# Kernel optimization log

Measured on AMD Instinct MI355X. Metric: run time of the kernel, lower is better.

## Reference

```python
import jax, jax.numpy as jnp
import numpy as np

N_ATOMS = 200_000
N_EDGES = 6_400_000  # ~32 neighbors/atom at 6A cutoff


def setup_inputs() -> dict:
    key = jax.random.key(0)
    k1, k2, k3, k4 = jax.random.split(key, 4)
    box_len = 60.0  # cubic cell edge (Angstrom) holding ~200k atoms
    pos = jax.random.uniform(k1, (N_ATOMS, 3), dtype=jnp.float32) * box_len
    # slightly triclinic periodic cell, batch of 1 structure
    box = (jnp.eye(3, dtype=jnp.float32) * box_len
           + jax.random.normal(k2, (3, 3), dtype=jnp.float32) * 0.5)[None]  # [1,3,3]
    edge_index = jax.random.randint(k3, (2, N_EDGES), 0, N_ATOMS, dtype=jnp.int32)
    shifts_idx = jax.random.randint(k4, (N_EDGES, 3), 0, 3, dtype=jnp.int32) - 1  # in {-1,0,1}
    batch_map = jnp.zeros((N_EDGES,), dtype=jnp.int32)  # single structure
    return {"pos": pos, "box": box, "edge_index": edge_index,
            "shifts_idx": shifts_idx, "batch_map": batch_map}


def reference(pos, box, edge_index, shifts_idx, batch_map):
    # compute_cell_shifts: per-edge shift vector = shifts_idx @ cell[batch]
    shifts_f = shifts_idx.astype(pos.dtype)                      # [E,3]
    cell_shifts = jnp.einsum('en,enm->em', shifts_f, box[batch_map])  # [E,3]
    # compute_distances + edge_vec (gather-based, periodic-corrected)
    dr = pos[edge_index[1]] - pos[edge_index[0]] + cell_shifts   # [E,3]
    edge_weight = jnp.linalg.norm(dr, axis=1)                    # [E]
    edge_vec = -dr                                               # [E,3]
    return edge_index, edge_weight, edge_vec, shifts_idx
```

## Files before the change

kernel.cpp:

```cpp
#include <hip/hip_runtime.h>


typedef int   vint4   __attribute__((ext_vector_type(4)));
typedef float vfloat4 __attribute__((ext_vector_type(4)));

struct f3 { float x, y, z; };

template <bool MULTI>
__global__ __launch_bounds__(256) void pd_kernel(
    const float* __restrict__ pos,
    const float* __restrict__ box,
    const int*   __restrict__ ei,
    const int*   __restrict__ sh,
    const int*   __restrict__ bmap,
    float* __restrict__ out,
    const long long E)
{
    const long long nG = E >> 2;
    float* out_ei = out;
    float* out_w  = out + 2 * E;
    float* out_v  = out + 3 * E;
    float* out_s  = out + 6 * E;

    float b00, b01, b02, b10, b11, b12, b20, b21, b22;
    if (!MULTI) {
        b00 = box[0]; b01 = box[1]; b02 = box[2];
        b10 = box[3]; b11 = box[4]; b12 = box[5];
        b20 = box[6]; b21 = box[7]; b22 = box[8];
    }

    const long long stride = (long long)gridDim.x * blockDim.x;

    for (long long g = (long long)blockIdx.x * blockDim.x + threadIdx.x;
         g < nG; g += stride) {
        const long long e0 = g << 2;

        const vint4 i4 = __builtin_nontemporal_load(
            reinterpret_cast<const vint4*>(ei + e0));
        const vint4 j4 = __builtin_nontemporal_load(
            reinterpret_cast<const vint4*>(ei + E + e0));
        const vint4 sA = __builtin_nontemporal_load(
            reinterpret_cast<const vint4*>(sh + 3 * e0));
        const vint4 sB = __builtin_nontemporal_load(
            reinterpret_cast<const vint4*>(sh + 3 * e0 + 4));
        const vint4 sC = __builtin_nontemporal_load(
            reinterpret_cast<const vint4*>(sh + 3 * e0 + 8));

        {
            vfloat4 t;
            t = (vfloat4){(float)i4.x, (float)i4.y, (float)i4.z, (float)i4.w};
            __builtin_nontemporal_store(t, reinterpret_cast<vfloat4*>(out_ei + e0));
            t = (vfloat4){(float)j4.x, (float)j4.y, (float)j4.z, (float)j4.w};
            __builtin_nontemporal_store(t, reinterpret_cast<vfloat4*>(out_ei + E + e0));
            t = (vfloat4){(float)sA.x, (float)sA.y, (float)sA.z, (float)sA.w};
            __builtin_nontemporal_store(t, reinterpret_cast<vfloat4*>(out_s + 3 * e0));
            t = (vfloat4){(float)sB.x, (float)sB.y, (float)sB.z, (float)sB.w};
            __builtin_nontemporal_store(t, reinterpret_cast<vfloat4*>(out_s + 3 * e0 + 4));
            t = (vfloat4){(float)sC.x, (float)sC.y, (float)sC.z, (float)sC.w};
            __builtin_nontemporal_store(t, reinterpret_cast<vfloat4*>(out_s + 3 * e0 + 8));
        }

        const int iv[4] = {i4.x, i4.y, i4.z, i4.w};
        const int jv[4] = {j4.x, j4.y, j4.z, j4.w};
        const int sv[12] = {sA.x, sA.y, sA.z, sA.w,
                            sB.x, sB.y, sB.z, sB.w,
                            sC.x, sC.y, sC.z, sC.w};
        int bv[4] = {0, 0, 0, 0};
        if (MULTI) {
            const vint4 b4 = __builtin_nontemporal_load(
                reinterpret_cast<const vint4*>(bmap + e0));
            bv[0] = b4.x; bv[1] = b4.y; bv[2] = b4.z; bv[3] = b4.w;
        }

        f3 pjv[4], piv[4];
#pragma unroll
        for (int k = 0; k < 4; ++k) {
            piv[k] = *reinterpret_cast<const f3*>(pos + 3LL * iv[k]);
            pjv[k] = *reinterpret_cast<const f3*>(pos + 3LL * jv[k]);
        }

        float w[4], v[12];
#pragma unroll
        for (int k = 0; k < 4; ++k) {
            float B00, B01, B02, B10, B11, B12, B20, B21, B22;
            if (MULTI) {
                const float* bb = box + 9LL * bv[k];
                B00 = bb[0]; B01 = bb[1]; B02 = bb[2];
                B10 = bb[3]; B11 = bb[4]; B12 = bb[5];
                B20 = bb[6]; B21 = bb[7]; B22 = bb[8];
            } else {
                B00 = b00; B01 = b01; B02 = b02;
                B10 = b10; B11 = b11; B12 = b12;
                B20 = b20; B21 = b21; B22 = b22;
            }
            const float sx = (float)sv[3 * k + 0];
            const float sy = (float)sv[3 * k + 1];
            const float sz = (float)sv[3 * k + 2];
            const float cx = sx * B00 + sy * B10 + sz * B20;
            const float cy = sx * B01 + sy * B11 + sz * B21;
            const float cz = sx * B02 + sy * B12 + sz * B22;

            const float dx = pjv[k].x - piv[k].x + cx;
            const float dy = pjv[k].y - piv[k].y + cy;
            const float dz = pjv[k].z - piv[k].z + cz;

            w[k] = sqrtf(dx * dx + dy * dy + dz * dz);
            v[3 * k + 0] = -dx;
            v[3 * k + 1] = -dy;
            v[3 * k + 2] = -dz;
        }

        __builtin_nontemporal_store(
            (vfloat4){w[0], w[1], w[2], w[3]},
            reinterpret_cast<vfloat4*>(out_w + e0));
        __builtin_nontemporal_store(
            (vfloat4){v[0], v[1], v[2], v[3]},
            reinterpret_cast<vfloat4*>(out_v + 3 * e0));
        __builtin_nontemporal_store(
            (vfloat4){v[4], v[5], v[6], v[7]},
            reinterpret_cast<vfloat4*>(out_v + 3 * e0 + 4));
        __builtin_nontemporal_store(
            (vfloat4){v[8], v[9], v[10], v[11]},
            reinterpret_cast<vfloat4*>(out_v + 3 * e0 + 8));
    }

    const long long tail0 = nG << 2;
    for (long long e = tail0 + (long long)blockIdx.x * blockDim.x + threadIdx.x;
         e < E; e += stride) {
        const int i = ei[e];
        const int j = ei[E + e];
        const int s0 = sh[3 * e], s1 = sh[3 * e + 1], s2 = sh[3 * e + 2];
        out_ei[e]     = (float)i;
        out_ei[E + e] = (float)j;
        out_s[3 * e]     = (float)s0;
        out_s[3 * e + 1] = (float)s1;
        out_s[3 * e + 2] = (float)s2;

        float B00, B01, B02, B10, B11, B12, B20, B21, B22;
        if (MULTI) {
            const float* bb = box + 9LL * bmap[e];
            B00 = bb[0]; B01 = bb[1]; B02 = bb[2];
            B10 = bb[3]; B11 = bb[4]; B12 = bb[5];
            B20 = bb[6]; B21 = bb[7]; B22 = bb[8];
        } else {
            B00 = b00; B01 = b01; B02 = b02;
            B10 = b10; B11 = b11; B12 = b12;
            B20 = b20; B21 = b21; B22 = b22;
        }
        const float sx = (float)s0, sy = (float)s1, sz = (float)s2;
        const float cx = sx * B00 + sy * B10 + sz * B20;
        const float cy = sx * B01 + sy * B11 + sz * B21;
        const float cz = sx * B02 + sy * B12 + sz * B22;
        const float dx = pos[3LL * j + 0] - pos[3LL * i + 0] + cx;
        const float dy = pos[3LL * j + 1] - pos[3LL * i + 1] + cy;
        const float dz = pos[3LL * j + 2] - pos[3LL * i + 2] + cz;
        out_w[e] = sqrtf(dx * dx + dy * dy + dz * dz);
        out_v[3 * e + 0] = -dx;
        out_v[3 * e + 1] = -dy;
        out_v[3 * e + 2] = -dz;
    }
}

extern "C" void kernel_launch(void* const* d_in, const int* in_sizes, int n_in,
                              void* d_out, int out_size, void* d_ws, size_t ws_size,
                              hipStream_t stream) {
    const float* pos  = (const float*)d_in[0];
    const float* box  = (const float*)d_in[1];
    const int*   ei   = (const int*)d_in[2];
    const int*   sh   = (const int*)d_in[3];
    const int*   bmap = (const int*)d_in[4];
    float* out = (float*)d_out;

    const long long E = (long long)in_sizes[4];
    const int n_struct = in_sizes[1] / 9;

    const int block = 256;
    long long nG = (E + 3) >> 2;
    long long blocks = (nG + block - 1) / block;
    if (blocks < 1) blocks = 1;
    if (blocks > 32768) blocks = 32768;

    if (n_struct == 1) {
        pd_kernel<false><<<(int)blocks, block, 0, stream>>>(
            pos, box, ei, sh, bmap, out, E);
    } else {
        pd_kernel<true><<<(int)blocks, block, 0, stream>>>(
            pos, box, ei, sh, bmap, out, E);
    }
}
```

Baseline: 371.1 us.

## Stage vector and shift outputs through LDS for fully coalesced stores

```diff
diff --git a/kernel.cpp b/kernel.cpp
--- a/kernel.cpp
+++ b/kernel.cpp
@@ -6,8 +6,12 @@
 
 struct f3 { float x, y, z; };
 
+#define BLOCK 256
+#define EPT   4
+#define EPB   (BLOCK * EPT)
+
 template <bool MULTI>
-__global__ __launch_bounds__(256) void pd_kernel(
+__global__ __launch_bounds__(BLOCK) void pd_kernel(
     const float* __restrict__ pos,
     const float* __restrict__ box,
     const int*   __restrict__ ei,
@@ -16,11 +20,15 @@
     float* __restrict__ out,
     const long long E)
 {
-    const long long nG = E >> 2;
+    __shared__ float lds[EPB * 3];
+
     float* out_ei = out;
     float* out_w  = out + 2 * E;
     float* out_v  = out + 3 * E;
     float* out_s  = out + 6 * E;
+
+    const int tid = threadIdx.x;
+    const long long E0 = (long long)blockIdx.x * EPB;
 
     float b00, b01, b02, b10, b11, b12, b20, b21, b22;
     if (!MULTI) {
@@ -29,42 +37,34 @@
         b20 = box[6]; b21 = box[7]; b22 = box[8];
     }
 
-    const long long stride = (long long)gridDim.x * blockDim.x;
-
-    for (long long g = (long long)blockIdx.x * blockDim.x + threadIdx.x;
-         g < nG; g += stride) {
-        const long long e0 = g << 2;
+    if (E0 + EPB <= E) {
+        const long long e0 = E0 + (long long)tid * EPT;
 
         const vint4 i4 = __builtin_nontemporal_load(
             reinterpret_cast<const vint4*>(ei + e0));
         const vint4 j4 = __builtin_nontemporal_load(
             reinterpret_cast<const vint4*>(ei + E + e0));
+        const int iv[4] = {i4.x, i4.y, i4.z, i4.w};
+        const int jv[4] = {j4.x, j4.y, j4.z, j4.w};
+
+        f3 piv[4], pjv[4];
+#pragma unroll
+        for (int k = 0; k < 4; ++k) {
+            piv[k] = *reinterpret_cast<const f3*>(pos + 3LL * iv[k]);
+            pjv[k] = *reinterpret_cast<const f3*>(pos + 3LL * jv[k]);
+        }
+
         const vint4 sA = __builtin_nontemporal_load(
             reinterpret_cast<const vint4*>(sh + 3 * e0));
         const vint4 sB = __builtin_nontemporal_load(
             reinterpret_cast<const vint4*>(sh + 3 * e0 + 4));
         const vint4 sC = __builtin_nontemporal_load(
             reinterpret_cast<const vint4*>(sh + 3 * e0 + 8));
-
-        {
-            vfloat4 t;
-            t = (vfloat4){(float)i4.x, (float)i4.y, (float)i4.z, (float)i4.w};
-            __builtin_nontemporal_store(t, reinterpret_cast<vfloat4*>(out_ei + e0));
-            t = (vfloat4){(float)j4.x, (float)j4.y, (float)j4.z, (float)j4.w};
-            __builtin_nontemporal_store(t, reinterpret_cast<vfloat4*>(out_ei + E + e0));
-            t = (vfloat4){(float)sA.x, (float)sA.y, (float)sA.z, (float)sA.w};
-            __builtin_nontemporal_store(t, reinterpret_cast<vfloat4*>(out_s + 3 * e0));
-            t = (vfloat4){(float)sB.x, (float)sB.y, (float)sB.z, (float)sB.w};
-            __builtin_nontemporal_store(t, reinterpret_cast<vfloat4*>(out_s + 3 * e0 + 4));
-            t = (vfloat4){(float)sC.x, (float)sC.y, (float)sC.z, (float)sC.w};
-            __builtin_nontemporal_store(t, reinterpret_cast<vfloat4*>(out_s + 3 * e0 + 8));
-        }
-
-        const int iv[4] = {i4.x, i4.y, i4.z, i4.w};
-        const int jv[4] = {j4.x, j4.y, j4.z, j4.w};
-        const int sv[12] = {sA.x, sA.y, sA.z, sA.w,
-                            sB.x, sB.y, sB.z, sB.w,
-                            sC.x, sC.y, sC.z, sC.w};
+        const float sf[12] = {
+            (float)sA.x, (float)sA.y, (float)sA.z, (float)sA.w,
+            (float)sB.x, (float)sB.y, (float)sB.z, (float)sB.w,
+            (float)sC.x, (float)sC.y, (float)sC.z, (float)sC.w};
+
         int bv[4] = {0, 0, 0, 0};
         if (MULTI) {
             const vint4 b4 = __builtin_nontemporal_load(
@@ -72,12 +72,12 @@
             bv[0] = b4.x; bv[1] = b4.y; bv[2] = b4.z; bv[3] = b4.w;
         }
 
-        f3 pjv[4], piv[4];
-#pragma unroll
-        for (int k = 0; k < 4; ++k) {
-            piv[k] = *reinterpret_cast<const f3*>(pos + 3LL * iv[k]);
-            pjv[k] = *reinterpret_cast<const f3*>(pos + 3LL * jv[k]);
-        }
+        __builtin_nontemporal_store(
+            (vfloat4){(float)i4.x, (float)i4.y, (float)i4.z, (float)i4.w},
+            reinterpret_cast<vfloat4*>(out_ei + e0));
+        __builtin_nontemporal_store(
+            (vfloat4){(float)j4.x, (float)j4.y, (float)j4.z, (float)j4.w},
+            reinterpret_cast<vfloat4*>(out_ei + E + e0));
 
         float w[4], v[12];
 #pragma unroll
@@ -93,9 +93,9 @@
                 B10 = b10; B11 = b11; B12 = b12;
                 B20 = b20; B21 = b21; B22 = b22;
             }
-            const float sx = (float)sv[3 * k + 0];
-            const float sy = (float)sv[3 * k + 1];
-            const float sz = (float)sv[3 * k + 2];
+            const float sx = sf[3 * k + 0];
+            const float sy = sf[3 * k + 1];
+            const float sz = sf[3 * k + 2];
             const float cx = sx * B00 + sy * B10 + sz * B20;
             const float cy = sx * B01 + sy * B11 + sz * B21;
             const float cz = sx * B02 + sy * B12 + sz * B22;
@@ -113,51 +113,73 @@
         __builtin_nontemporal_store(
             (vfloat4){w[0], w[1], w[2], w[3]},
             reinterpret_cast<vfloat4*>(out_w + e0));
-        __builtin_nontemporal_store(
-            (vfloat4){v[0], v[1], v[2], v[3]},
-            reinterpret_cast<vfloat4*>(out_v + 3 * e0));
-        __builtin_nontemporal_store(
-            (vfloat4){v[4], v[5], v[6], v[7]},
-            reinterpret_cast<vfloat4*>(out_v + 3 * e0 + 4));
-        __builtin_nontemporal_store(
-            (vfloat4){v[8], v[9], v[10], v[11]},
-            reinterpret_cast<vfloat4*>(out_v + 3 * e0 + 8));
-    }
-
-    const long long tail0 = nG << 2;
-    for (long long e = tail0 + (long long)blockIdx.x * blockDim.x + threadIdx.x;
-         e < E; e += stride) {
-        const int i = ei[e];
-        const int j = ei[E + e];
-        const int s0 = sh[3 * e], s1 = sh[3 * e + 1], s2 = sh[3 * e + 2];
-        out_ei[e]     = (float)i;
-        out_ei[E + e] = (float)j;
-        out_s[3 * e]     = (float)s0;
-        out_s[3 * e + 1] = (float)s1;
-        out_s[3 * e + 2] = (float)s2;
-
-        float B00, B01, B02, B10, B11, B12, B20, B21, B22;
-        if (MULTI) {
-            const float* bb = box + 9LL * bmap[e];
-            B00 = bb[0]; B01 = bb[1]; B02 = bb[2];
-            B10 = bb[3]; B11 = bb[4]; B12 = bb[5];
-            B20 = bb[6]; B21 = bb[7]; B22 = bb[8];
-        } else {
-            B00 = b00; B01 = b01; B02 = b02;
-            B10 = b10; B11 = b11; B12 = b12;
-            B20 = b20; B21 = b21; B22 = b22;
-        }
-        const float sx = (float)s0, sy = (float)s1, sz = (float)s2;
-        const float cx = sx * B00 + sy * B10 + sz * B20;
-        const float cy = sx * B01 + sy * B11 + sz * B21;
-        const float cz = sx * B02 + sy * B12 + sz * B22;
-        const float dx = pos[3LL * j + 0] - pos[3LL * i + 0] + cx;
-        const float dy = pos[3LL * j + 1] - pos[3LL * i + 1] + cy;
-        const float dz = pos[3LL * j + 2] - pos[3LL * i + 2] + cz;
-        out_w[e] = sqrtf(dx * dx + dy * dy + dz * dz);
-        out_v[3 * e + 0] = -dx;
-        out_v[3 * e + 1] = -dy;
-        out_v[3 * e + 2] = -dz;
+
+        {
+            vfloat4* lrow = reinterpret_cast<vfloat4*>(&lds[tid * 12]);
+            lrow[0] = (vfloat4){v[0], v[1], v[2], v[3]};
+            lrow[1] = (vfloat4){v[4], v[5], v[6], v[7]};
+            lrow[2] = (vfloat4){v[8], v[9], v[10], v[11]};
+        }
+        __syncthreads();
+#pragma unroll
+        for (int q = 0; q < 3; ++q) {
+            const int idx = tid + BLOCK * q;
+            const vfloat4 val =
+                *reinterpret_cast<const vfloat4*>(&lds[idx * 4]);
+            __builtin_nontemporal_store(
+                val, reinterpret_cast<vfloat4*>(out_v + 3 * E0 + 4LL * idx));
+        }
+        __syncthreads();
+
+        {
+            vfloat4* lrow = reinterpret_cast<vfloat4*>(&lds[tid * 12]);
+            lrow[0] = (vfloat4){sf[0], sf[1], sf[2], sf[3]};
+            lrow[1] = (vfloat4){sf[4], sf[5], sf[6], sf[7]};
+            lrow[2] = (vfloat4){sf[8], sf[9], sf[10], sf[11]};
+        }
+        __syncthreads();
+#pragma unroll
+        for (int q = 0; q < 3; ++q) {
+            const int idx = tid + BLOCK * q;
+            const vfloat4 val =
+                *reinterpret_cast<const vfloat4*>(&lds[idx * 4]);
+            __builtin_nontemporal_store(
+                val, reinterpret_cast<vfloat4*>(out_s + 3 * E0 + 4LL * idx));
+        }
+    } else {
+        for (long long e = E0 + tid; e < E; e += BLOCK) {
+            const int i = ei[e];
+            const int j = ei[E + e];
+            const int s0 = sh[3 * e], s1 = sh[3 * e + 1], s2 = sh[3 * e + 2];
+            out_ei[e]     = (float)i;
+            out_ei[E + e] = (float)j;
+            out_s[3 * e]     = (float)s0;
+            out_s[3 * e + 1] = (float)s1;
+            out_s[3 * e + 2] = (float)s2;
+
+            float B00, B01, B02, B10, B11, B12, B20, B21, B22;
+            if (MULTI) {
+                const float* bb = box + 9LL * bmap[e];
+                B00 = bb[0]; B01 = bb[1]; B02 = bb[2];
+                B10 = bb[3]; B11 = bb[4]; B12 = bb[5];
+                B20 = bb[6]; B21 = bb[7]; B22 = bb[8];
+            } else {
+                B00 = b00; B01 = b01; B02 = b02;
+                B10 = b10; B11 = b11; B12 = b12;
+                B20 = b20; B21 = b21; B22 = b22;
+            }
+            const float sx = (float)s0, sy = (float)s1, sz = (float)s2;
+            const float cx = sx * B00 + sy * B10 + sz * B20;
+            const float cy = sx * B01 + sy * B11 + sz * B21;
+            const float cz = sx * B02 + sy * B12 + sz * B22;
+            const float dx = pos[3LL * j + 0] - pos[3LL * i + 0] + cx;
+            const float dy = pos[3LL * j + 1] - pos[3LL * i + 1] + cy;
+            const float dz = pos[3LL * j + 2] - pos[3LL * i + 2] + cz;
+            out_w[e] = sqrtf(dx * dx + dy * dy + dz * dz);
+            out_v[3 * e + 0] = -dx;
+            out_v[3 * e + 1] = -dy;
+            out_v[3 * e + 2] = -dz;
+        }
     }
 }
 
@@ -174,17 +196,14 @@
     const long long E = (long long)in_sizes[4];
     const int n_struct = in_sizes[1] / 9;
 
-    const int block = 256;
-    long long nG = (E + 3) >> 2;
-    long long blocks = (nG + block - 1) / block;
+    long long blocks = (E + EPB - 1) / EPB;
     if (blocks < 1) blocks = 1;
-    if (blocks > 32768) blocks = 32768;
 
     if (n_struct == 1) {
-        pd_kernel<false><<<(int)blocks, block, 0, stream>>>(
+        pd_kernel<false><<<(int)blocks, BLOCK, 0, stream>>>(
             pos, box, ei, sh, bmap, out, E);
     } else {
-        pd_kernel<true><<<(int)blocks, block, 0, stream>>>(
+        pd_kernel<true><<<(int)blocks, BLOCK, 0, stream>>>(
             pos, box, ei, sh, bmap, out, E);
     }
 }
```

Measured after the change: 371.9 us. No clear change (+0.2%).
